# Kernel tuning notes

Measured on AMD Instinct MI355X. Metric: run time of the kernel, lower is better.

Reference implementation:

```python
import jax, jax.numpy as jnp
import numpy as np

B, C, H, W = 4, 256, 64, 64
TOPK = 3
RAT_S = 0.05  # rat_s passed in Corr.forward


def _zero_window_mask(h, w, rat_s=RAT_S):
    # mask[m, i, j] = 1 - gaussian centered at pixel m=(m//w, m%w); sigma=(h*rat_s, w*rat_s)
    sr, sc = h * rat_s, w * rat_s
    r = jnp.arange(h, dtype=jnp.float32)
    c = jnp.arange(w, dtype=jnp.float32)
    cent_r = jnp.repeat(r, w)  # [hw]
    cent_c = jnp.tile(c, h)    # [hw]
    g = (jnp.exp(-((r[None, :, None] - cent_r[:, None, None]) ** 2) / (2.0 * sr * sr))
         * jnp.exp(-((c[None, None, :] - cent_c[:, None, None]) ** 2) / (2.0 * sc * sc)))
    return (1.0 - g).reshape(h * w, h * w)


def setup_inputs() -> dict:
    key = jax.random.key(0)
    x = jax.random.normal(key, (B, C, H, W), dtype=jnp.float32)
    alpha = jnp.asarray(5.0, dtype=jnp.float32)  # learned scalar nn.Parameter
    return {"x": x, "alpha": alpha}


def reference(x, alpha):
    b, c, h, w = x.shape
    # F.normalize(x, p=2, dim=-3): L2-normalize channels with eps clamp
    nrm = jnp.linalg.norm(x, axis=1, keepdims=True)
    xn = x / jnp.maximum(nrm, 1e-12)
    xf = xn.reshape(b, c, h * w)
    # correlation GEMM: [b, hw, hw]
    aff = jnp.einsum('bcm,bcn->bmn', xf, xf)
    aff = aff * _zero_window_mask(h, w)[None]
    s = aff * alpha
    xc = jax.nn.softmax(s, axis=-1) * jax.nn.softmax(s, axis=-2)
    # topk over the source-pixel dim (dim=-3 of [b, hw, h, w])
    xc = xc.reshape(b, h * w, h, w).transpose(0, 2, 3, 1)  # [b, h, w, hw]
    val, _ = jax.lax.top_k(xc, TOPK)                        # [b, h, w, k]
    return val.transpose(0, 3, 1, 2)                        # [b, k, h, w]
```

## Files before the change

### kernel.cpp

```cpp
#include <hip/hip_runtime.h>
#include <hip/hip_bf16.h>
#include <math.h>


#define HW 4096
#define CDIM 256
#define INV2S2 0.048828125f
#define NEGINF -1e30f
#define NTILE 528
#define LOG2E 1.4426950408889634f

#if defined(__has_builtin)
#  if __has_builtin(__builtin_amdgcn_exp2f)
#    define EXP2F(x) __builtin_amdgcn_exp2f(x)
#  else
#    define EXP2F(x) exp2f(x)
#  endif
#else
#  define EXP2F(x) exp2f(x)
#endif

typedef __bf16 bf16;
typedef _Float16 f16;
typedef __attribute__((ext_vector_type(8))) __bf16 bf16x8;
typedef __attribute__((ext_vector_type(4))) _Float16 f16x4;
typedef __attribute__((ext_vector_type(4))) float f32x4;

#define GAS __attribute__((address_space(1)))
#define LAS __attribute__((address_space(3)))

__device__ __forceinline__ void ins3(float v, float& t0, float& t1, float& t2) {
    float n0 = fmaxf(t0, v);
    float n1 = __builtin_amdgcn_fmed3f(t0, t1, v);
    float n2 = __builtin_amdgcn_fmed3f(t1, t2, v);
    t0 = n0; t1 = n1; t2 = n2;
}

__device__ __forceinline__ void decode_tri(int t, int& mt, int& nt) {
    int m = (int)((sqrtf(8.f * (float)t + 1.f) - 1.f) * 0.5f);
    while ((m + 1) * (m + 2) / 2 <= t) ++m;
    while (m * (m + 1) / 2 > t) --m;
    mt = m;
    nt = t - m * (m + 1) / 2;
}

__global__ __launch_bounds__(256) void corr_norm(const float* __restrict__ x,
                                                 bf16* __restrict__ xnT) {
    __shared__ float red[4][64];
    __shared__ float invn[64];
    __shared__ __align__(16) bf16 T[64][264];
    int tid = threadIdx.x;
    int pl = tid & 63, cg = tid >> 6;
    int P0 = blockIdx.x * 64;
    int P = P0 + pl;
    int b = P >> 12;
    int pix = P & 4095;
    const float* xb = x + ((size_t)(b * CDIM + cg * 64) << 12) + pix;
    float v[64];
    float ss = 0.f;
#pragma unroll
    for (int j = 0; j < 64; ++j) {
        v[j] = xb[(size_t)j << 12];
        ss += v[j] * v[j];
    }
    red[cg][pl] = ss;
    __syncthreads();
    if (tid < 64) {
        float s = red[0][tid] + red[1][tid] + red[2][tid] + red[3][tid];
        invn[tid] = 1.0f / fmaxf(sqrtf(s), 1e-12f);
    }
    __syncthreads();
    float inv = invn[pl];
#pragma unroll
    for (int j0 = 0; j0 < 64; j0 += 8) {
        bf16x8 pk;
#pragma unroll
        for (int j = 0; j < 8; ++j) pk[j] = (bf16)(v[j0 + j] * inv);
        *(bf16x8*)(&T[pl][cg * 64 + j0]) = pk;
    }
    __syncthreads();
#pragma unroll
    for (int it = 0; it < 8; ++it) {
        int p = it * 8 + (tid >> 5);
        int k = tid & 31;
        bf16x8 val = *(const bf16x8*)(&T[p][k * 8]);
        *(bf16x8*)(xnT + (size_t)(P0 + p) * CDIM + k * 8) = val;
    }
}

__device__ __forceinline__ void build_ext(float* extw, int lane, int adr, float scale) {
    float fr2 = (float)(adr * adr);
#pragma unroll
    for (int h = 0; h < 2; ++h) {
        int j = lane + h * 64;
        float d = (float)(j - 63);
        extw[j] = scale * (1.f - __expf(-(fr2 + d * d) * INV2S2));
    }
}

__device__ __forceinline__ void load_etab(const float* extw_wave, int quad, int l15,
                                          float (&e)[7][4]) {
    const float* p = extw_wave + 63 + quad * 4 - l15;
#pragma unroll
    for (int dm = 0; dm < 7; ++dm)
#pragma unroll
        for (int r = 0; r < 4; ++r) e[dm][r] = p[(dm - 3) * 16 + r];
}

__global__ __launch_bounds__(256) void corr_rowsum(const bf16* __restrict__ xnT,
                                                   const float* __restrict__ alpha_p,
                                                   float* __restrict__ rpart,
                                                   f16* __restrict__ sbuf,
                                                   int store_s2) {
    __shared__ __align__(16) bf16 SH[16384];
    __shared__ float F[1024];
    bf16* As = SH;
    bf16* Bs = SH + 8192;
    int tid = threadIdx.x;
    int lin = blockIdx.x;
    int xcd = lin & 7;
    int b = xcd >> 1;
    int pr = ((lin >> 3) << 1) + (xcd & 1);
    int wave = tid >> 6, lane = tid & 63;
    int wm = wave >> 1, wn = wave & 1, l15 = lane & 15, quad = lane >> 4;
    float alpha2 = alpha_p[0] * LOG2E;
    const bf16* xb = xnT + ((size_t)b << 20);
    const int rslot = ((quad + (l15 >> 1)) & 3) * 8;

    int mt0, nt0, mt1, nt1;
    decode_tri(2 * pr, mt0, nt0);
    decode_tri(2 * pr + 1, mt1, nt1);

    auto issue = [&](int mbase, int nbase, int kk, int buf) {
#pragma unroll
        for (int r = 0; r < 2; ++r) {
            int idx = r * 256 + tid;
            int prow = idx >> 2;
            int sub = ((idx & 3) - (prow >> 1)) & 3;
            const bf16* gA = xb + ((size_t)(mbase + prow) << 8) + kk * 32 + (sub << 3);
            const bf16* gB = xb + ((size_t)(nbase + prow) << 8) + kk * 32 + (sub << 3);
            bf16* lA = As + buf * 4096 + ((r * 4 + wave) << 9);
            bf16* lB = Bs + buf * 4096 + ((r * 4 + wave) << 9);
            __builtin_amdgcn_global_load_lds((const GAS void*)gA, (LAS void*)lA, 16, 0, 0);
            __builtin_amdgcn_global_load_lds((const GAS void*)gB, (LAS void*)lB, 16, 0, 0);
        }
    };

    issue(mt0 * 128, nt0 * 128, 0, 0);

    for (int tile = 0; tile < 2; ++tile) {
        const int mt = tile ? mt1 : mt0;
        const int nt = tile ? nt1 : nt0;
        const int t = 2 * pr + tile;
        const int mbase = mt * 128, nbase = nt * 128;

        f32x4 acc[4][4];
#pragma unroll
        for (int mi = 0; mi < 4; ++mi)
#pragma unroll
            for (int ni = 0; ni < 4; ++ni) acc[mi][ni] = (f32x4)0.f;

#pragma unroll
        for (int kk = 0; kk < 8; ++kk) {
            __syncthreads();
            if (kk < 7)
                issue(mbase, nbase, kk + 1, (kk + 1) & 1);
            else if (tile == 0)
                issue(mt1 * 128, nt1 * 128, 0, 0);
            int buf = kk & 1;
            bf16x8 af[4], bfr[4];
#pragma unroll
            for (int i = 0; i < 4; ++i) {
                af[i]  = *(const bf16x8*)(As + buf * 4096 + (wm * 64 + i * 16 + l15) * 32 + rslot);
                bfr[i] = *(const bf16x8*)(Bs + buf * 4096 + (wn * 64 + i * 16 + l15) * 32 + rslot);
            }
#pragma unroll
            for (int mi = 0; mi < 4; ++mi)
#pragma unroll
                for (int ni = 0; ni < 4; ++ni)
                    acc[mi][ni] = __builtin_amdgcn_mfma_f32_16x16x32_bf16(af[mi], bfr[ni],
                                                                          acc[mi][ni], 0, 0, 0);
        }

        int rowi = (mbase + wm * 64) >> 6;
        int coli = (nbase + wn * 64) >> 6;
        int adr = rowi - coli; if (adr < 0) adr = -adr;
        float* ext  = F;
        float* rbuf = F + 512;
        float* cbuf = F + 768;
        build_ext(ext + wave * 128, lane, adr, alpha2);
        float e[7][4];
        load_etab(ext + wave * 128, quad, l15, e);

        const size_t tb = (size_t)(b * NTILE + t) * 16384;
        float colpart[4] = {0.f, 0.f, 0.f, 0.f};
#pragma unroll
        for (int mi = 0; mi < 4; ++mi) {
#pragma unroll
            for (int r = 0; r < 4; ++r) {
                float ssum = 0.f;
                float sv[4];
#pragma unroll
                for (int ni = 0; ni < 4; ++ni) {
                    float p = e[mi - ni + 3][r] * acc[mi][ni][r];
                    sv[ni] = p;
                    float ev = EXP2F(p);
                    ssum += ev;
                    colpart[ni] += ev;
                }
                if (store_s2) {
                    f16x4 pk;
#pragma unroll
                    for (int ni = 0; ni < 4; ++ni) pk[ni] = (f16)(sv[ni] + sv[ni]);
                    *(f16x4*)(sbuf + tb + (mi * 4 + r) * 1024 + tid * 4) = pk;
                }
                ssum += __shfl_xor(ssum, 1);
                ssum += __shfl_xor(ssum, 2);
                ssum += __shfl_xor(ssum, 4);
                ssum += __shfl_xor(ssum, 8);
                if (l15 == 0) rbuf[wn * 128 + wm * 64 + mi * 16 + quad * 4 + r] = ssum;
            }
        }
#pragma unroll
        for (int ni = 0; ni < 4; ++ni) {
            float c = colpart[ni];
            c += __shfl_xor(c, 16);
            c += __shfl_xor(c, 32);
            if (quad == 0) cbuf[wm * 128 + wn * 64 + ni * 16 + l15] = c;
        }
        __syncthreads();
        if (tid < 128) {
            rpart[(size_t)((b * 32 + mt) * 32 + nt) * 128 + tid] = rbuf[tid] + rbuf[128 + tid];
        } else if (mt != nt) {
            int j = tid - 128;
            rpart[(size_t)((b * 32 + nt) * 32 + mt) * 128 + j] = cbuf[j] + cbuf[128 + j];
        }
    }
}

__global__ __launch_bounds__(256) void corr_recip(const float* __restrict__ rpart,
                                                  float* __restrict__ ism,
                                                  float* __restrict__ lsm) {
    int i = blockIdx.x * 256 + threadIdx.x;
    if (i >= 4 * HW) return;
    int b = i >> 12, gr = i & 4095, s = gr >> 7, j = gr & 127;
    const float* base = rpart + (size_t)((b * 32 + s) * 32) * 128 + j;
    float sum = 0.f;
#pragma unroll
    for (int sl = 0; sl < 32; ++sl) sum += base[sl * 128];
    ism[i] = 1.0f / sum;
    lsm[i] = -log2f(sum);
}

__device__ __forceinline__ void topk_epilogue(int b, int mt, int nt,
                                              const float (&s2f)[16][4],
                                              const float (&lr)[4][4], const float (&lc)[4],
                                              float* mbuf, float* rtop,
                                              float* __restrict__ wtop,
                                              int tid, int wm, int wn, int l15, int quad) {
#pragma unroll
    for (int ni = 0; ni < 4; ++ni) {
        float t0 = NEGINF, t1 = NEGINF, t2 = NEGINF;
#pragma unroll
        for (int mi = 0; mi < 4; ++mi) {
#pragma unroll
            for (int r = 0; r < 4; ++r) {
                float key = s2f[mi * 4 + r][ni] + lr[mi][r];
                ins3(key, t0, t1, t2);
            }
        }
#pragma unroll
        for (int d = 16; d <= 32; d <<= 1) {
            float s0 = __shfl_xor(t0, d);
            float s1 = __shfl_xor(t1, d);
            float s2 = __shfl_xor(t2, d);
            ins3(s0, t0, t1, t2);
            ins3(s1, t0, t1, t2);
            ins3(s2, t0, t1, t2);
        }
        if (quad == 0) {
            int cl = wn * 64 + ni * 16 + l15;
            mbuf[(wm * 128 + cl) * 3 + 0] = t0;
            mbuf[(wm * 128 + cl) * 3 + 1] = t1;
            mbuf[(wm * 128 + cl) * 3 + 2] = t2;
        }
    }
    __syncthreads();
    if (mt != nt) {
#pragma unroll
        for (int mi = 0; mi < 4; ++mi) {
#pragma unroll
            for (int r = 0; r < 4; ++r) {
                float u0 = NEGINF, u1 = NEGINF, u2 = NEGINF;
#pragma unroll
                for (int ni = 0; ni < 4; ++ni) {
                    float key = s2f[mi * 4 + r][ni] + lc[ni];
                    ins3(key, u0, u1, u2);
                }
                {
                    float s0 = __shfl_xor(u0, 8);
                    float s1 = __shfl_xor(u1, 8);
                    float s2 = __shfl_xor(u2, 8);
                    ins3(s0, u0, u1, u2);
                    ins3(s1, u0, u1, u2);
                    ins3(s2, u0, u1, u2);
                }
                if (l15 < 8) {
                    int row = wm * 64 + mi * 16 + quad * 4 + r;
                    int slot = wn * 8 + l15;
                    float* q = rtop + row * 51 + slot * 3;
                    q[0] = u0; q[1] = u1; q[2] = u2;
                }
            }
        }
    }
    __syncthreads();
    if (tid < 128) {
        float t0 = mbuf[tid * 3], t1 = mbuf[tid * 3 + 1], t2 = mbuf[tid * 3 + 2];
        ins3(mbuf[(128 + tid) * 3 + 0], t0, t1, t2);
        ins3(mbuf[(128 + tid) * 3 + 1], t0, t1, t2);
        ins3(mbuf[(128 + tid) * 3 + 2], t0, t1, t2);
        size_t o = ((size_t)((b * 32 + nt) * 32 + mt) * 128 + tid) * 3;
        wtop[o] = t0;
        wtop[o + 1] = t1;
        wtop[o + 2] = t2;
        if (mt != nt) {
            float v0 = NEGINF, v1 = NEGINF, v2 = NEGINF;
            const float* q = rtop + tid * 51;
#pragma unroll
            for (int sl = 0; sl < 16; ++sl) {
                ins3(q[sl * 3 + 0], v0, v1, v2);
                ins3(q[sl * 3 + 1], v0, v1, v2);
                ins3(q[sl * 3 + 2], v0, v1, v2);
            }
            size_t o2 = ((size_t)((b * 32 + mt) * 32 + nt) * 128 + tid) * 3;
            wtop[o2] = v0;
            wtop[o2 + 1] = v1;
            wtop[o2 + 2] = v2;
        }
    }
}

__global__ __launch_bounds__(256) void corr_topsel(const f16* __restrict__ sbuf,
                                                   const float* __restrict__ lsm,
                                                   float* __restrict__ wtop) {
    __shared__ float FS[7296];
    float* mbuf = FS;
    float* rtop = FS + 768;
    int tid = threadIdx.x;
    int lin = blockIdx.x;
    int xcd = lin & 7;
    int b = xcd >> 1;
    int t = ((lin >> 3) << 1) + (xcd & 1);
    int mt, nt;
    decode_tri(t, mt, nt);
    int mbase = mt * 128, nbase = nt * 128;
    int wave = tid >> 6, lane = tid & 63;
    int wm = wave >> 1, wn = wave & 1, l15 = lane & 15, quad = lane >> 4;

    const size_t tb = (size_t)(b * NTILE + t) * 16384;
    float s2f[16][4];
#pragma unroll
    for (int k = 0; k < 16; ++k) {
        f16x4 hv = *(const f16x4*)(sbuf + tb + k * 1024 + tid * 4);
#pragma unroll
        for (int ni = 0; ni < 4; ++ni) s2f[k][ni] = (float)hv[ni];
    }
    float lr[4][4];
#pragma unroll
    for (int mi = 0; mi < 4; ++mi)
#pragma unroll
        for (int r = 0; r < 4; ++r)
            lr[mi][r] = lsm[(b << 12) + mbase + wm * 64 + mi * 16 + quad * 4 + r];
    float lc[4];
#pragma unroll
    for (int ni = 0; ni < 4; ++ni)
        lc[ni] = lsm[(b << 12) + nbase + wn * 64 + ni * 16 + l15];

    topk_epilogue(b, mt, nt, s2f, lr, lc, mbuf, rtop, wtop, tid, wm, wn, l15, quad);
}

__global__ __launch_bounds__(256) void corr_topk(const bf16* __restrict__ xnT,
                                                 const float* __restrict__ alpha_p,
                                                 const float* __restrict__ lsm,
                                                 float* __restrict__ wtop) {
    __shared__ __align__(16) bf16 SH[16384];
    bf16* As = SH;
    bf16* Bs = SH + 8192;
    int tid = threadIdx.x;
    int lin = blockIdx.x;
    int xcd = lin & 7;
    int b = xcd >> 1;
    int t = ((lin >> 3) << 1) + (xcd & 1);
    int mt, nt;
    decode_tri(t, mt, nt);
    int mbase = mt * 128, nbase = nt * 128;
    int wave = tid >> 6, lane = tid & 63;
    int wm = wave >> 1, wn = wave & 1, l15 = lane & 15, quad = lane >> 4;
    int rowi = (mbase + wm * 64) >> 6;
    int coli = (nbase + wn * 64) >> 6;
    int adr = rowi - coli; if (adr < 0) adr = -adr;
    float a2 = 2.0f * alpha_p[0] * LOG2E;
    const bf16* xb = xnT + ((size_t)b << 20);
    const int rslot = ((quad + (l15 >> 1)) & 3) * 8;

    auto issue = [&](int kk, int buf) {
#pragma unroll
        for (int r = 0; r < 2; ++r) {
            int idx = r * 256 + tid;
            int prow = idx >> 2;
            int sub = ((idx & 3) - (prow >> 1)) & 3;
            const bf16* gA = xb + ((size_t)(mbase + prow) << 8) + kk * 32 + (sub << 3);
            const bf16* gB = xb + ((size_t)(nbase + prow) << 8) + kk * 32 + (sub << 3);
            bf16* lA = As + buf * 4096 + ((r * 4 + wave) << 9);
            bf16* lB = Bs + buf * 4096 + ((r * 4 + wave) << 9);
            __builtin_amdgcn_global_load_lds((const GAS void*)gA, (LAS void*)lA, 16, 0, 0);
            __builtin_amdgcn_global_load_lds((const GAS void*)gB, (LAS void*)lB, 16, 0, 0);
        }
    };

    f32x4 acc[4][4];
#pragma unroll
    for (int mi = 0; mi < 4; ++mi)
#pragma unroll
        for (int ni = 0; ni < 4; ++ni) acc[mi][ni] = (f32x4)0.f;
    issue(0, 0);
#pragma unroll
    for (int kk = 0; kk < 8; ++kk) {
        __syncthreads();
        if (kk < 7) issue(kk + 1, (kk + 1) & 1);
        int buf = kk & 1;
        bf16x8 af[4], bfr[4];
#pragma unroll
        for (int i = 0; i < 4; ++i) {
            af[i]  = *(const bf16x8*)(As + buf * 4096 + (wm * 64 + i * 16 + l15) * 32 + rslot);
            bfr[i] = *(const bf16x8*)(Bs + buf * 4096 + (wn * 64 + i * 16 + l15) * 32 + rslot);
        }
#pragma unroll
        for (int mi = 0; mi < 4; ++mi)
#pragma unroll
            for (int ni = 0; ni < 4; ++ni)
                acc[mi][ni] = __builtin_amdgcn_mfma_f32_16x16x32_bf16(af[mi], bfr[ni],
                                                                      acc[mi][ni], 0, 0, 0);
    }

    float* Fh = (float*)SH;
    float* ext  = Fh;
    float* mbuf = Fh + 512;
    float* rtop = Fh + 1280;
    build_ext(ext + wave * 128, lane, adr, a2);
    float e[7][4];
    load_etab(ext + wave * 128, quad, l15, e);

    float s2f[16][4];
#pragma unroll
    for (int mi = 0; mi < 4; ++mi)
#pragma unroll
        for (int r = 0; r < 4; ++r)
#pragma unroll
            for (int ni = 0; ni < 4; ++ni)
                s2f[mi * 4 + r][ni] = e[mi - ni + 3][r] * acc[mi][ni][r];
    float lr[4][4];
#pragma unroll
    for (int mi = 0; mi < 4; ++mi)
#pragma unroll
        for (int r = 0; r < 4; ++r)
            lr[mi][r] = lsm[(b << 12) + mbase + wm * 64 + mi * 16 + quad * 4 + r];
    float lc[4];
#pragma unroll
    for (int ni = 0; ni < 4; ++ni)
        lc[ni] = lsm[(b << 12) + nbase + wn * 64 + ni * 16 + l15];

    __syncthreads();
    topk_epilogue(b, mt, nt, s2f, lr, lc, mbuf, rtop, wtop, tid, wm, wn, l15, quad);
}

__global__ __launch_bounds__(256) void corr_merge(const float* __restrict__ wtop,
                                                  const float* __restrict__ ism,
                                                  float* __restrict__ out) {
    int idx = blockIdx.x * 256 + threadIdx.x;
    if (idx >= 4 * HW) return;
    int b = idx >> 12, col = idx & 4095;
    int strip = col >> 7, j = col & 127;
    const float* base = wtop + ((size_t)((b * 32 + strip) * 32) * 128 + j) * 3;
    float t0 = NEGINF, t1 = NEGINF, t2 = NEGINF;
    for (int sl = 0; sl < 32; ++sl) {
        const float* q = base + (size_t)sl * 128 * 3;
        ins3(q[0], t0, t1, t2);
        ins3(q[1], t0, t1, t2);
        ins3(q[2], t0, t1, t2);
    }
    float ismc = ism[idx];
    out[((b * 3 + 0) << 12) + col] = EXP2F(t0) * ismc;
    out[((b * 3 + 1) << 12) + col] = EXP2F(t1) * ismc;
    out[((b * 3 + 2) << 12) + col] = EXP2F(t2) * ismc;
}

extern "C" void kernel_launch(void* const* d_in, const int* in_sizes, int n_in,
                              void* d_out, int out_size, void* d_ws, size_t ws_size,
                              hipStream_t stream) {
    const float* x = (const float*)d_in[0];
    const float* alpha = (const float*)d_in[1];
    float* out = (float*)d_out;
    char* ws = (char*)d_ws;
    bf16* xnT = (bf16*)ws;
    float* ism = (float*)(ws + (8u << 20));
    float* lsm = (float*)(ws + (8u << 20) + (64u << 10));
    float* rpart = (float*)(ws + (8u << 20) + (128u << 10));
    float* wtop  = (float*)(ws + (8u << 20) + (128u << 10));
    f16* sbuf = (f16*)(ws + (8u << 20) + (128u << 10) + (6u << 20));
    size_t need = (8u << 20) + (128u << 10) + (6u << 20) + (size_t)4 * NTILE * 16384 * 2;
    int fast = (ws_size >= need);

    corr_norm<<<256, 256, 0, stream>>>(x, xnT);
    corr_rowsum<<<NTILE * 2, 256, 0, stream>>>(xnT, alpha, rpart, sbuf, fast);
    corr_recip<<<64, 256, 0, stream>>>(rpart, ism, lsm);
    if (fast)
        corr_topsel<<<NTILE * 4, 256, 0, stream>>>(sbuf, lsm, wtop);
    else
        corr_topk<<<NTILE * 4, 256, 0, stream>>>(xnT, alpha, lsm, wtop);
    corr_merge<<<64, 256, 0, stream>>>(wtop, ism, out);
}
```

Before: 149.2 us.

## Split rowsum GEMM tiles into half-row blocks for more parallelism

The row-sum kernel no longer processes two 128x128 triangle tiles per block. Each block now computes one 64x128 half tile, giving four times as many blocks, with smaller LDS use and fewer accumulators. The row-partial layout doubles so that each half writes its own slot, and the reciprocal kernel sums 64 partials instead of 32. The topsel kernel also switches to nontemporal loads of the stored scores. The cost is that B-operand loads are repeated across the two halves and the previous prefetch overlap between consecutive tiles is gone.

```diff
diff --git a/kernel.cpp b/kernel.cpp
--- a/kernel.cpp
+++ b/kernel.cpp
@@ -112,129 +112,135 @@
                                                    float* __restrict__ rpart,
                                                    f16* __restrict__ sbuf,
                                                    int store_s2) {
-    __shared__ __align__(16) bf16 SH[16384];
-    __shared__ float F[1024];
+    __shared__ __align__(16) bf16 SH[12288];
     bf16* As = SH;
-    bf16* Bs = SH + 8192;
+    bf16* Bs = SH + 4096;
     int tid = threadIdx.x;
     int lin = blockIdx.x;
     int xcd = lin & 7;
     int b = xcd >> 1;
-    int pr = ((lin >> 3) << 1) + (xcd & 1);
+    int v = lin >> 3;
+    int h = v & 1;
+    int t = ((v >> 1) << 1) + (xcd & 1);
+    int mt, nt;
+    decode_tri(t, mt, nt);
+    int mbase = mt * 128 + h * 64;
+    int nbase = nt * 128;
     int wave = tid >> 6, lane = tid & 63;
     int wm = wave >> 1, wn = wave & 1, l15 = lane & 15, quad = lane >> 4;
+    int rowi = mbase >> 6;
+    int coli = (nbase + wn * 64) >> 6;
+    int adr = rowi - coli; if (adr < 0) adr = -adr;
     float alpha2 = alpha_p[0] * LOG2E;
     const bf16* xb = xnT + ((size_t)b << 20);
     const int rslot = ((quad + (l15 >> 1)) & 3) * 8;
 
-    int mt0, nt0, mt1, nt1;
-    decode_tri(2 * pr, mt0, nt0);
-    decode_tri(2 * pr + 1, mt1, nt1);
-
-    auto issue = [&](int mbase, int nbase, int kk, int buf) {
+    auto issue = [&](int kk, int buf) {
+        {
+            int idx = tid;
+            int prow = idx >> 2;
+            int sub = ((idx & 3) - (prow >> 1)) & 3;
+            const bf16* gA = xb + ((size_t)(mbase + prow) << 8) + kk * 32 + (sub << 3);
+            bf16* lA = As + buf * 2048 + (wave << 9);
+            __builtin_amdgcn_global_load_lds((const GAS void*)gA, (LAS void*)lA, 16, 0, 0);
+        }
 #pragma unroll
         for (int r = 0; r < 2; ++r) {
             int idx = r * 256 + tid;
             int prow = idx >> 2;
             int sub = ((idx & 3) - (prow >> 1)) & 3;
-            const bf16* gA = xb + ((size_t)(mbase + prow) << 8) + kk * 32 + (sub << 3);
             const bf16* gB = xb + ((size_t)(nbase + prow) << 8) + kk * 32 + (sub << 3);
-            bf16* lA = As + buf * 4096 + ((r * 4 + wave) << 9);
             bf16* lB = Bs + buf * 4096 + ((r * 4 + wave) << 9);
-            __builtin_amdgcn_global_load_lds((const GAS void*)gA, (LAS void*)lA, 16, 0, 0);
             __builtin_amdgcn_global_load_lds((const GAS void*)gB, (LAS void*)lB, 16, 0, 0);
         }
     };
 
-    issue(mt0 * 128, nt0 * 128, 0, 0);
-
-    for (int tile = 0; tile < 2; ++tile) {
-        const int mt = tile ? mt1 : mt0;
-        const int nt = tile ? nt1 : nt0;
-        const int t = 2 * pr + tile;
-        const int mbase = mt * 128, nbase = nt * 128;
-
-        f32x4 acc[4][4];
-#pragma unroll
-        for (int mi = 0; mi < 4; ++mi)
-#pragma unroll
-            for (int ni = 0; ni < 4; ++ni) acc[mi][ni] = (f32x4)0.f;
-
-#pragma unroll
-        for (int kk = 0; kk < 8; ++kk) {
-            __syncthreads();
-            if (kk < 7)
-                issue(mbase, nbase, kk + 1, (kk + 1) & 1);
-            else if (tile == 0)
-                issue(mt1 * 128, nt1 * 128, 0, 0);
-            int buf = kk & 1;
-            bf16x8 af[4], bfr[4];
-#pragma unroll
-            for (int i = 0; i < 4; ++i) {
-                af[i]  = *(const bf16x8*)(As + buf * 4096 + (wm * 64 + i * 16 + l15) * 32 + rslot);
-                bfr[i] = *(const bf16x8*)(Bs + buf * 4096 + (wn * 64 + i * 16 + l15) * 32 + rslot);
+    f32x4 acc[2][4];
+#pragma unroll
+    for (int mi = 0; mi < 2; ++mi)
+#pragma unroll
+        for (int ni = 0; ni < 4; ++ni) acc[mi][ni] = (f32x4)0.f;
+
+    issue(0, 0);
+#pragma unroll
+    for (int kk = 0; kk < 8; ++kk) {
+        __syncthreads();
+        if (kk < 7) issue(kk + 1, (kk + 1) & 1);
+        int buf = kk & 1;
+        bf16x8 af[2], bfr[4];
+#pragma unroll
+        for (int i = 0; i < 2; ++i)
+            af[i] = *(const bf16x8*)(As + buf * 2048 + (wm * 32 + i * 16 + l15) * 32 + rslot);
+#pragma unroll
+        for (int i = 0; i < 4; ++i)
+            bfr[i] = *(const bf16x8*)(Bs + buf * 4096 + (wn * 64 + i * 16 + l15) * 32 + rslot);
+#pragma unroll
+        for (int mi = 0; mi < 2; ++mi)
+#pragma unroll
+            for (int ni = 0; ni < 4; ++ni)
+                acc[mi][ni] = __builtin_amdgcn_mfma_f32_16x16x32_bf16(af[mi], bfr[ni],
+                                                                      acc[mi][ni], 0, 0, 0);
+    }
+
+    float* F = (float*)SH;
+    float* ext  = F;
+    float* rbuf = F + 512;
+    float* cbuf = F + 640;
+    build_ext(ext + wave * 128, lane, adr, alpha2);
+    float e[5][4];
+    {
+        const float* p = ext + wave * 128 + 63 + wm * 32 + quad * 4 - l15;
+#pragma unroll
+        for (int dm = 0; dm < 5; ++dm)
+#pragma unroll
+            for (int r = 0; r < 4; ++r) e[dm][r] = p[(dm - 3) * 16 + r];
+    }
+
+    const size_t tb = (size_t)(b * NTILE + t) * 16384;
+    float colpart[4] = {0.f, 0.f, 0.f, 0.f};
+#pragma unroll
+    for (int mi = 0; mi < 2; ++mi) {
+#pragma unroll
+        for (int r = 0; r < 4; ++r) {
+            float ssum = 0.f;
+            float sv[4];
+#pragma unroll
+            for (int ni = 0; ni < 4; ++ni) {
+                float p = e[mi - ni + 3][r] * acc[mi][ni][r];
+                sv[ni] = p;
+                float ev = EXP2F(p);
+                ssum += ev;
+                colpart[ni] += ev;
             }
-#pragma unroll
-            for (int mi = 0; mi < 4; ++mi)
-#pragma unroll
-                for (int ni = 0; ni < 4; ++ni)
-                    acc[mi][ni] = __builtin_amdgcn_mfma_f32_16x16x32_bf16(af[mi], bfr[ni],
-                                                                          acc[mi][ni], 0, 0, 0);
-        }
-
-        int rowi = (mbase + wm * 64) >> 6;
-        int coli = (nbase + wn * 64) >> 6;
-        int adr = rowi - coli; if (adr < 0) adr = -adr;
-        float* ext  = F;
-        float* rbuf = F + 512;
-        float* cbuf = F + 768;
-        build_ext(ext + wave * 128, lane, adr, alpha2);
-        float e[7][4];
-        load_etab(ext + wave * 128, quad, l15, e);
-
-        const size_t tb = (size_t)(b * NTILE + t) * 16384;
-        float colpart[4] = {0.f, 0.f, 0.f, 0.f};
-#pragma unroll
-        for (int mi = 0; mi < 4; ++mi) {
-#pragma unroll
-            for (int r = 0; r < 4; ++r) {
-                float ssum = 0.f;
-                float sv[4];
-#pragma unroll
-                for (int ni = 0; ni < 4; ++ni) {
-                    float p = e[mi - ni + 3][r] * acc[mi][ni][r];
-                    sv[ni] = p;
-                    float ev = EXP2F(p);
-                    ssum += ev;
-                    colpart[ni] += ev;
-                }
-                if (store_s2) {
-                    f16x4 pk;
-#pragma unroll
-                    for (int ni = 0; ni < 4; ++ni) pk[ni] = (f16)(sv[ni] + sv[ni]);
-                    *(f16x4*)(sbuf + tb + (mi * 4 + r) * 1024 + tid * 4) = pk;
-                }
-                ssum += __shfl_xor(ssum, 1);
-                ssum += __shfl_xor(ssum, 2);
-                ssum += __shfl_xor(ssum, 4);
-                ssum += __shfl_xor(ssum, 8);
-                if (l15 == 0) rbuf[wn * 128 + wm * 64 + mi * 16 + quad * 4 + r] = ssum;
+            if (store_s2) {
+                f16x4 pk;
+#pragma unroll
+                for (int ni = 0; ni < 4; ++ni) pk[ni] = (f16)(sv[ni] + sv[ni]);
+                *(f16x4*)(sbuf + tb + ((wm * 2 + mi) * 4 + r) * 1024 +
+                          ((h * 2 + wn) * 64 + lane) * 4) = pk;
             }
-        }
-#pragma unroll
-        for (int ni = 0; ni < 4; ++ni) {
-            float c = colpart[ni];
-            c += __shfl_xor(c, 16);
-            c += __shfl_xor(c, 32);
-            if (quad == 0) cbuf[wm * 128 + wn * 64 + ni * 16 + l15] = c;
-        }
-        __syncthreads();
-        if (tid < 128) {
-            rpart[(size_t)((b * 32 + mt) * 32 + nt) * 128 + tid] = rbuf[tid] + rbuf[128 + tid];
-        } else if (mt != nt) {
-            int j = tid - 128;
-            rpart[(size_t)((b * 32 + nt) * 32 + mt) * 128 + j] = cbuf[j] + cbuf[128 + j];
-        }
+            ssum += __shfl_xor(ssum, 1);
+            ssum += __shfl_xor(ssum, 2);
+            ssum += __shfl_xor(ssum, 4);
+            ssum += __shfl_xor(ssum, 8);
+            if (l15 == 0) rbuf[wn * 64 + wm * 32 + mi * 16 + quad * 4 + r] = ssum;
+        }
+    }
+#pragma unroll
+    for (int ni = 0; ni < 4; ++ni) {
+        float c = colpart[ni];
+        c += __shfl_xor(c, 16);
+        c += __shfl_xor(c, 32);
+        if (quad == 0) cbuf[wm * 128 + wn * 64 + ni * 16 + l15] = c;
+    }
+    __syncthreads();
+    if (tid < 128) {
+        int j = tid;
+        float vr = ((j >> 6) == h) ? (rbuf[j & 63] + rbuf[64 + (j & 63)]) : 0.f;
+        rpart[(size_t)((b * 32 + mt) * 64 + nt * 2 + h) * 128 + j] = vr;
+    } else if (mt != nt) {
+        int j = tid - 128;
+        rpart[(size_t)((b * 32 + nt) * 64 + mt * 2 + h) * 128 + j] = cbuf[j] + cbuf[128 + j];
     }
 }
 
@@ -244,10 +250,10 @@
     int i = blockIdx.x * 256 + threadIdx.x;
     if (i >= 4 * HW) return;
     int b = i >> 12, gr = i & 4095, s = gr >> 7, j = gr & 127;
-    const float* base = rpart + (size_t)((b * 32 + s) * 32) * 128 + j;
+    const float* base = rpart + (size_t)((b * 32 + s) * 64) * 128 + j;
     float sum = 0.f;
 #pragma unroll
-    for (int sl = 0; sl < 32; ++sl) sum += base[sl * 128];
+    for (int sl = 0; sl < 64; ++sl) sum += base[sl * 128];
     ism[i] = 1.0f / sum;
     lsm[i] = -log2f(sum);
 }
@@ -362,7 +368,7 @@
     float s2f[16][4];
 #pragma unroll
     for (int k = 0; k < 16; ++k) {
-        f16x4 hv = *(const f16x4*)(sbuf + tb + k * 1024 + tid * 4);
+        f16x4 hv = __builtin_nontemporal_load((const f16x4*)(sbuf + tb + k * 1024 + tid * 4));
 #pragma unroll
         for (int ni = 0; ni < 4; ++ni) s2f[k][ni] = (float)hv[ni];
     }
@@ -513,7 +519,7 @@
     int fast = (ws_size >= need);
 
     corr_norm<<<256, 256, 0, stream>>>(x, xnT);
-    corr_rowsum<<<NTILE * 2, 256, 0, stream>>>(xnT, alpha, rpart, sbuf, fast);
+    corr_rowsum<<<NTILE * 8, 256, 0, stream>>>(xnT, alpha, rpart, sbuf, fast);
     corr_recip<<<64, 256, 0, stream>>>(rpart, ism, lsm);
     if (fast)
         corr_topsel<<<NTILE * 4, 256, 0, stream>>>(sbuf, lsm, wtop);
```

Result: faster. 131.4 us, median of 2 (-11.9%).
